# Optimization experiments

Hardware: AMD Instinct MI355X
Metric: run time of the kernel (lower is better)

Reference implementation:

```python
import jax, jax.numpy as jnp
import numpy as np

D = 1024      # embedding_dim
H = 16        # num_heads
DH = D // H   # head_dim
DFF = 4 * D
EPS = 1e-5


def setup_inputs() -> dict:
    key = jax.random.key(0)
    ks = jax.random.split(key, 10)
    B, T = 2, 2048
    s = 0.02
    return {
        "x": jax.random.normal(ks[0], (B, T, D), dtype=jnp.float32),
        "Wq": jax.random.normal(ks[1], (H, D, DH), dtype=jnp.float32) * s,
        "Wk": jax.random.normal(ks[2], (H, D, DH), dtype=jnp.float32) * s,
        "Wv": jax.random.normal(ks[3], (H, D, DH), dtype=jnp.float32) * s,
        "W1": jax.random.normal(ks[4], (D, DFF), dtype=jnp.float32) * s,
        "b1": jnp.zeros((DFF,), dtype=jnp.float32),
        "W2": jax.random.normal(ks[5], (DFF, D), dtype=jnp.float32) * s,
        "b2": jnp.zeros((D,), dtype=jnp.float32),
        "gamma1": jnp.ones((D,), dtype=jnp.float32),
        "beta1": jnp.zeros((D,), dtype=jnp.float32),
        "gamma2": jnp.ones((D,), dtype=jnp.float32),
        "beta2": jnp.zeros((D,), dtype=jnp.float32),
    }


def _layernorm(x, gamma, beta):
    # torch.var default is unbiased (ddof=1) -- faithful to LayerNorm1d
    mean = jnp.mean(x, axis=-1, keepdims=True)
    var = jnp.var(x, axis=-1, keepdims=True, ddof=1)
    return gamma * (x - mean) * jax.lax.rsqrt(var + EPS) + beta


def _block(x, Wq, Wk, Wv, W1, b1, W2, b2, gamma1, beta1, gamma2, beta2):
    B, T, _ = x.shape
    h = _layernorm(x, gamma1, beta1)
    # per-head projections stacked: [B,H,T,DH]
    Q = jnp.einsum('btd,hde->bhte', h, Wq)
    K = jnp.einsum('btd,hde->bhte', h, Wk)
    V = jnp.einsum('btd,hde->bhte', h, Wv)
    # NOTE: original scales by 1/sqrt(embedding_dim), NOT head_dim
    scores = jnp.einsum('bhqe,bhke->bhqk', Q, K) / jnp.sqrt(jnp.float32(D))
    causal = jnp.tril(jnp.ones((T, T), dtype=bool))
    scores = jnp.where(causal, scores, -jnp.inf)
    attn = jax.nn.softmax(scores, axis=-1)
    out = jnp.einsum('bhqk,bhke->bhqe', attn, V)
    # torch.cat over heads along last dim == transpose+reshape
    out = out.transpose(0, 2, 1, 3).reshape(B, T, D)
    x = x + out
    h2 = _layernorm(x, gamma2, beta2)
    ff = jax.nn.relu(h2 @ W1 + b1) @ W2 + b2  # dropout is identity at inference
    return x + ff


def reference(x, Wq, Wk, Wv, W1, b1, W2, b2, gamma1, beta1, gamma2, beta2):
    return _block(x, Wq, Wk, Wv, W1, b1, W2, b2, gamma1, beta1, gamma2, beta2)
```

## Files before the change

kernel.cpp:

```cpp
#include <hip/hip_runtime.h>

typedef unsigned short u16;
typedef __bf16 bf16;
typedef __attribute__((ext_vector_type(8))) __bf16 bf16x8;
typedef __attribute__((ext_vector_type(4))) float f32x4;
typedef __attribute__((ext_vector_type(8))) unsigned short u16x8;
typedef unsigned long long u64;

__device__ __forceinline__ float bf2f(u16 h) {
  return __uint_as_float(((unsigned int)h) << 16);
}
__device__ __forceinline__ u16 f2bf(float f) {
  unsigned int u = __float_as_uint(f);
  return (u16)((u + 0x7fffu + ((u >> 16) & 1u)) >> 16);
}
__device__ __forceinline__ u16 ld_cv(const void* p, size_t i, int f32) {
  return f32 ? f2bf(((const float*)p)[i]) : ((const u16*)p)[i];
}
__device__ __forceinline__ float ld_f(const void* p, size_t i, int f32) {
  return f32 ? ((const float*)p)[i] : bf2f(((const u16*)p)[i]);
}
__device__ __forceinline__ void async16(const u16* g, u16* l) {
  __builtin_amdgcn_global_load_lds(
      (const __attribute__((address_space(1))) unsigned int*)g,
      (__attribute__((address_space(3))) unsigned int*)l, 16, 0, 0);
}
__device__ __forceinline__ float exp2_raw(float x) {
  float r;
  asm("v_exp_f32 %0, %1" : "=v"(r) : "v"(x));
  return r;
}
__device__ __forceinline__ unsigned cvt_pk_bf16(float a, float b) {
  unsigned r;
  asm("v_cvt_pk_bf16_f32 %0, %1, %2" : "=v"(r) : "v"(a), "v"(b));
  return r;
}

__global__ void prep_kernel(const u16* __restrict__ x,
                            const void* __restrict__ Wq, const void* __restrict__ Wk,
                            const void* __restrict__ Wv, const void* __restrict__ W1,
                            const void* __restrict__ W2,
                            u16* __restrict__ WTq, u16* __restrict__ W1T,
                            u16* __restrict__ W2T,
                            const void* __restrict__ gamma1,
                            const void* __restrict__ beta1,
                            u16* __restrict__ hOut, int* __restrict__ flag) {
  __shared__ u16 tile[64][65];
  __shared__ int sm[4];
  __shared__ float ss[4], ssq[4];
  const int tid = threadIdx.x;
  int me = 0;
#pragma unroll
  for (int j = 0; j < 4; j++) {
    const u16 v = x[(tid * 4 + j) * 2];
    const int e = (v >> 7) & 0xFF;
    me = me > e ? me : e;
  }
#pragma unroll
  for (int off = 32; off > 0; off >>= 1) {
    const int o = __shfl_down(me, off);
    me = me > o ? me : o;
  }
  if ((tid & 63) == 0) sm[tid >> 6] = me;
  __syncthreads();
  const int a01 = sm[0] > sm[1] ? sm[0] : sm[1];
  const int a23 = sm[2] > sm[3] ? sm[2] : sm[3];
  const int f = ((a01 > a23 ? a01 : a23) >= 140) ? 1 : 0;
  if (blockIdx.x == 0 && tid == 0) *flag = f;

  const int bid = blockIdx.x;
  if (bid >= 2816) {
    const size_t row = bid - 2816;
    float v0, v1, v2, v3;
    if (f) {
      const float4 v = *((const float4*)x + row * 256 + tid);
      v0 = v.x; v1 = v.y; v2 = v.z; v3 = v.w;
    } else {
      const ushort4 u = *((const ushort4*)x + row * 256 + tid);
      v0 = bf2f(u.x); v1 = bf2f(u.y); v2 = bf2f(u.z); v3 = bf2f(u.w);
    }
    float s = v0 + v1 + v2 + v3;
    float sq = v0 * v0 + v1 * v1 + v2 * v2 + v3 * v3;
#pragma unroll
    for (int off = 32; off > 0; off >>= 1) {
      s += __shfl_down(s, off);
      sq += __shfl_down(sq, off);
    }
    if ((tid & 63) == 0) { ss[tid >> 6] = s; ssq[tid >> 6] = sq; }
    __syncthreads();
    s = ss[0] + ss[1] + ss[2] + ss[3];
    sq = ssq[0] + ssq[1] + ssq[2] + ssq[3];
    const float mean = s * (1.f / 1024.f);
    const float var = (sq - 1024.f * mean * mean) * (1.f / 1023.f);
    const float rs = rsqrtf(var + 1e-5f);
    const int c0 = tid * 4;
    ushort4 o;
    o.x = f2bf(ld_f(gamma1, c0 + 0, f) * (v0 - mean) * rs + ld_f(beta1, c0 + 0, f));
    o.y = f2bf(ld_f(gamma1, c0 + 1, f) * (v1 - mean) * rs + ld_f(beta1, c0 + 1, f));
    o.z = f2bf(ld_f(gamma1, c0 + 2, f) * (v2 - mean) * rs + ld_f(beta1, c0 + 2, f));
    o.w = f2bf(ld_f(gamma1, c0 + 3, f) * (v3 - mean) * rs + ld_f(beta1, c0 + 3, f));
    *(ushort4*)&hOut[row * 1024 + tid * 4] = o;
    return;
  }

  const void* src;
  u16* dst;
  int R, C, tcc, trr, rowbase;
  size_t sb = 0;
  if (bid < 768) {
    const int bx = bid & 15, wh = bid >> 4;
    const int w = wh >> 4, hh = wh & 15;
    trr = bx * 64;
    src = (w == 0) ? Wq : ((w == 1) ? Wk : Wv);
    sb = (size_t)hh * 65536;
    dst = WTq; R = 1024; C = 64; tcc = 0;
    rowbase = w * 1024 + hh * 64;
  } else if (bid < 1792) {
    const int j = bid - 768;
    src = W1; dst = W1T; R = 1024; C = 4096;
    tcc = (j & 63) * 64; trr = (j >> 6) * 64;
    rowbase = tcc;
  } else {
    const int j = bid - 1792;
    src = W2; dst = W2T; R = 4096; C = 1024;
    tcc = (j & 15) * 64; trr = (j >> 4) * 64;
    rowbase = tcc;
  }
  const int rr = tid >> 4, c4 = (tid & 15) * 4;
#pragma unroll
  for (int p = 0; p < 4; p++) {
    const int r = p * 16 + rr;
    const size_t off = sb + (size_t)(trr + r) * C + tcc + c4;
    if (f) {
      const float4 v = *(const float4*)((const float*)src + off);
      tile[r][c4 + 0] = f2bf(v.x);
      tile[r][c4 + 1] = f2bf(v.y);
      tile[r][c4 + 2] = f2bf(v.z);
      tile[r][c4 + 3] = f2bf(v.w);
    } else {
      const ushort4 u = *(const ushort4*)((const u16*)src + off);
      tile[r][c4 + 0] = u.x;
      tile[r][c4 + 1] = u.y;
      tile[r][c4 + 2] = u.z;
      tile[r][c4 + 3] = u.w;
    }
  }
  __syncthreads();
#pragma unroll
  for (int p = 0; p < 4; p++) {
    const int wrow = p * 16 + rr;
    ushort4 o;
    o.x = tile[c4 + 0][wrow];
    o.y = tile[c4 + 1][wrow];
    o.z = tile[c4 + 2][wrow];
    o.w = tile[c4 + 3][wrow];
    *(ushort4*)&dst[(size_t)(rowbase + wrow) * R + trr + c4] = o;
  }
}

template <int EPI, int WR, int WC, bool MS>
__launch_bounds__(WR * WC * 64)
__global__ void gemm_bt(const u16* __restrict__ A, const u16* __restrict__ B,
                        int K, int KLD, int NX, int N,
                        const void* __restrict__ bias, const u16* __restrict__ res,
                        void* __restrict__ out,
                        u16* __restrict__ Qo, u16* __restrict__ Ko, u16* __restrict__ Vto,
                        const int* __restrict__ flag) {
  constexpr int BM = WR * 64, BN = WC * 64, T = WR * WC * 64;
  constexpr int RPA = T / 4;
  constexpr int RAH = BM / RPA;
  constexpr int RBH = BN / RPA;
  __shared__ __align__(16) u16 As[BM * 64];
  __shared__ __align__(16) u16 Bs[BN * 64];
  const int tid = threadIdx.x;
  const int bid = blockIdx.x;
  const int sxp = NX >> 3;
  const int xcd = bid & 7, j9 = bid >> 3;
  int m0, n0;
  if (MS) {
    m0 = (xcd * sxp + j9 % sxp) * BM;
    n0 = (j9 / sxp) * BN;
  } else {
    n0 = (xcd * sxp + j9 % sxp) * BN;
    m0 = (j9 / sxp) * BM;
  }
  const int wave = tid >> 6, lane = tid & 63;
  const int wm = (wave / WC) * 64, wn = (wave % WC) * 64;
  const int lm = lane & 15, lq = lane >> 4;
  const int fb = (EPI == 1 || EPI == 2) ? *flag : 0;

  const f32x4 zero = {0.f, 0.f, 0.f, 0.f};
  f32x4 acc[4][4];
#pragma unroll
  for (int i = 0; i < 4; i++)
#pragma unroll
    for (int j = 0; j < 4; j++) acc[i][j] = zero;

  const int ar = tid >> 2;
  const int ac = ((tid & 3) ^ ((tid >> 3) & 3)) * 8;
  const u16* Ag = A + (size_t)(m0 + ar) * KLD + ac;
  const u16* Bg = B + (size_t)(n0 + ar) * KLD + ac;
  u16* AsP = &As[tid * 8];
  u16* BsP = &Bs[tid * 8];
  const int rq = (lq ^ ((lm >> 1) & 3)) * 8;

  for (int k0 = 0; k0 < K; k0 += 64) {
#pragma unroll
    for (int hh = 0; hh < 2; hh++) {
#pragma unroll
      for (int c = 0; c < RAH; c++)
        async16(Ag + k0 + hh * 32 + (size_t)c * RPA * KLD,
                AsP + hh * BM * 32 + c * RPA * 32);
#pragma unroll
      for (int c = 0; c < RBH; c++)
        async16(Bg + k0 + hh * 32 + (size_t)c * RPA * KLD,
                BsP + hh * BN * 32 + c * RPA * 32);
    }
    __syncthreads();
    bf16x8 a0[4], a1[4], b0[4], b1[4];
#pragma unroll
    for (int i = 0; i < 4; i++) {
      a0[i] = *(const bf16x8*)&As[(wm + i * 16 + lm) * 32 + rq];
      a1[i] = *(const bf16x8*)&As[BM * 32 + (wm + i * 16 + lm) * 32 + rq];
    }
#pragma unroll
    for (int i = 0; i < 4; i++) {
      b0[i] = *(const bf16x8*)&Bs[(wn + i * 16 + lm) * 32 + rq];
      b1[i] = *(const bf16x8*)&Bs[BN * 32 + (wn + i * 16 + lm) * 32 + rq];
    }
#pragma unroll
    for (int i = 0; i < 4; i++)
#pragma unroll
      for (int j = 0; j < 4; j++) {
        acc[i][j] = __builtin_amdgcn_mfma_f32_16x16x32_bf16(a0[i], b0[j], acc[i][j], 0, 0, 0);
        acc[i][j] = __builtin_amdgcn_mfma_f32_16x16x32_bf16(a1[i], b1[j], acc[i][j], 0, 0, 0);
      }
    __syncthreads();
  }

  if (EPI == 0) {
#pragma unroll
    for (int i = 0; i < 4; i++) {
      const int row0 = m0 + wm + i * 16 + lq * 4;
      const int bb = row0 >> 11, t0 = row0 & 2047;
#pragma unroll
      for (int j = 0; j < 4; j++) {
        const int col = n0 + wn + j * 16 + lm;
        const int w = col >> 10, nn = col & 1023;
        const int hh = nn >> 6, e = nn & 63;
        if (w == 2) {
          ushort4 v4;
          v4.x = f2bf(acc[i][j][0]);
          v4.y = f2bf(acc[i][j][1]);
          v4.z = f2bf(acc[i][j][2]);
          v4.w = f2bf(acc[i][j][3]);
          *(ushort4*)&Vto[(((size_t)(bb * 16 + hh)) * 64 + e) * 2048 + t0] = v4;
        } else {
          u16* dst = (w == 0) ? Qo : Ko;
          const float qs = (w == 0) ? 0.04508422f : 1.0f;
#pragma unroll
          for (int r = 0; r < 4; r++)
            dst[(((size_t)(bb * 16 + hh)) * 2048 + t0 + r) * 64 + e] =
                f2bf(acc[i][j][r] * qs);
        }
      }
    }
  } else {
#pragma unroll
    for (int i = 0; i < 4; i++) {
#pragma unroll
      for (int r = 0; r < 4; r++) {
        const int row = m0 + wm + i * 16 + lq * 4 + r;
#pragma unroll
        for (int j = 0; j < 4; j++) {
          const int col = n0 + wn + j * 16 + lm;
          const float c = acc[i][j][r];
          if (EPI == 1) {
            const float v = c + ld_f(bias, col, fb);
            ((u16*)out)[(size_t)row * N + col] = f2bf(v > 0.f ? v : 0.f);
          } else {
            const float v = c + ld_f(bias, col, fb) + bf2f(res[(size_t)row * N + col]);
            if (fb)
              ((float*)out)[(size_t)row * N + col] = v;
            else
              ((u16*)out)[(size_t)row * N + col] = f2bf(v);
          }
        }
      }
    }
  }
}

__launch_bounds__(512)
__global__ void gemm_sk2(const u16* __restrict__ A, const u16* __restrict__ B,
                         u16* __restrict__ P0, u16* __restrict__ P1) {
  __shared__ __align__(16) unsigned char smem[66560];
  const int tid = threadIdx.x;
  const int bid = blockIdx.x;
  const int xcd = bid & 7, j9 = bid >> 3;
  const int m0 = (xcd * 4 + (j9 & 3)) * 128;
  const int n0 = ((j9 >> 2) & 7) * 128;
  const int khb = (j9 >> 5) & 1;
  const int wave = tid >> 6, lane = tid & 63;
  const int g = wave >> 2, lw = wave & 3;
  const int gtid = tid & 255;
  const int wm = (lw >> 1) * 64, wn = (lw & 1) * 64;
  const int lm = lane & 15, lq = lane >> 4;

  const f32x4 zero = {0.f, 0.f, 0.f, 0.f};
  f32x4 acc[4][4];
#pragma unroll
  for (int i = 0; i < 4; i++)
#pragma unroll
    for (int j = 0; j < 4; j++) acc[i][j] = zero;

  const int ar = gtid >> 2;
  const int ac = ((gtid & 3) ^ ((gtid >> 3) & 3)) * 8;
  const int koff = khb * 2048 + g * 1024;
  const u16* Ag = A + (size_t)(m0 + ar) * 4096 + koff + ac;
  const u16* Bg = B + (size_t)(n0 + ar) * 4096 + koff + ac;
  u16* Sg = (u16*)smem + g * 16384;
  u16* AsP = &Sg[gtid * 8];
  u16* BsP = &Sg[8192 + gtid * 8];
  const int rq = (lq ^ ((lm >> 1) & 3)) * 8;

  for (int k0 = 0; k0 < 1024; k0 += 64) {
#pragma unroll
    for (int hh = 0; hh < 2; hh++) {
#pragma unroll
      for (int c = 0; c < 2; c++) {
        async16(Ag + k0 + hh * 32 + (size_t)c * 64 * 4096,
                AsP + hh * 4096 + c * 2048);
        async16(Bg + k0 + hh * 32 + (size_t)c * 64 * 4096,
                BsP + hh * 4096 + c * 2048);
      }
    }
    __syncthreads();
    bf16x8 a0[4], a1[4], b0[4], b1[4];
#pragma unroll
    for (int i = 0; i < 4; i++) {
      a0[i] = *(const bf16x8*)&Sg[(wm + i * 16 + lm) * 32 + rq];
      a1[i] = *(const bf16x8*)&Sg[4096 + (wm + i * 16 + lm) * 32 + rq];
    }
#pragma unroll
    for (int i = 0; i < 4; i++) {
      b0[i] = *(const bf16x8*)&Sg[8192 + (wn + i * 16 + lm) * 32 + rq];
      b1[i] = *(const bf16x8*)&Sg[8192 + 4096 + (wn + i * 16 + lm) * 32 + rq];
    }
#pragma unroll
    for (int i = 0; i < 4; i++)
#pragma unroll
      for (int j = 0; j < 4; j++) {
        acc[i][j] = __builtin_amdgcn_mfma_f32_16x16x32_bf16(a0[i], b0[j], acc[i][j], 0, 0, 0);
        acc[i][j] = __builtin_amdgcn_mfma_f32_16x16x32_bf16(a1[i], b1[j], acc[i][j], 0, 0, 0);
      }
    __syncthreads();
  }

  float* Ml = (float*)smem;
  if (g == 1) {
#pragma unroll
    for (int i = 0; i < 4; i++)
#pragma unroll
      for (int j = 0; j < 4; j++)
#pragma unroll
        for (int r = 0; r < 4; r++)
          Ml[(wm + i * 16 + lq * 4 + r) * 130 + wn + j * 16 + lm] = acc[i][j][r];
  }
  __syncthreads();
  if (g == 0) {
    u16* P = khb ? P1 : P0;
#pragma unroll
    for (int i = 0; i < 4; i++) {
#pragma unroll
      for (int r = 0; r < 4; r++) {
        const int row = m0 + wm + i * 16 + lq * 4 + r;
#pragma unroll
        for (int j = 0; j < 4; j++) {
          const int col = n0 + wn + j * 16 + lm;
          const float v = acc[i][j][r] +
                          Ml[(wm + i * 16 + lq * 4 + r) * 130 + wn + j * 16 + lm];
          P[(size_t)row * 1024 + col] = f2bf(v);
        }
      }
    }
  }
}

__launch_bounds__(256)
__global__ void ffn2_reduce(const u16* __restrict__ P0, const u16* __restrict__ P1,
                            const void* __restrict__ bias, const u16* __restrict__ res,
                            void* __restrict__ out, const int* __restrict__ flag) {
  const int f = *flag;
  const size_t i0 = ((size_t)blockIdx.x * 256 + threadIdx.x) * 8;
  const int col = (int)(i0 & 1023);
  const u16x8 a8 = *(const u16x8*)(P0 + i0);
  const u16x8 b8 = *(const u16x8*)(P1 + i0);
  const u16x8 r8 = *(const u16x8*)(res + i0);
  float v[8];
#pragma unroll
  for (int k = 0; k < 8; k++)
    v[k] = bf2f(a8[k]) + bf2f(b8[k]) + ld_f(bias, col + k, f) + bf2f(r8[k]);
  if (f) {
    float4 o0 = {v[0], v[1], v[2], v[3]};
    float4 o1 = {v[4], v[5], v[6], v[7]};
    *(float4*)((float*)out + i0) = o0;
    *(float4*)((float*)out + i0 + 4) = o1;
  } else {
    u16x8 o8;
#pragma unroll
    for (int k = 0; k < 8; k++) o8[k] = f2bf(v[k]);
    *(u16x8*)((u16*)out + i0) = o8;
  }
}

__launch_bounds__(256)
__global__ void attn_mfma(const u16* __restrict__ Q, const u16* __restrict__ K,
                          const u16* __restrict__ Vt, const void* __restrict__ xres,
                          const int* __restrict__ flag, u16* __restrict__ x2) {
  __shared__ __align__(16) unsigned char smem[35328];
  const int tid = threadIdx.x;
  const int wave = tid >> 6, lane = tid & 63;
  const int lm = lane & 15, quad = lane >> 4;
  const int bid = blockIdx.x;
  const int xcd = bid & 7, jj = bid >> 3;
  const int bh = xcd + 8 * (jj & 3);
  const int pair = jj >> 2;
  const int b = bh >> 4, h = bh & 15;
  const int f32in = *flag;

  u16* stw = (u16*)smem + wave * 4096;
  u16* Ksw = stw;
  u16* Vsw = stw + 2048;
  float (*Olds)[32][68] = (float(*)[32][68])smem;
  float (*Llds)[2][16] = (float(*)[2][16])(smem + 34816);

  const u16* Kbh = K + (size_t)bh * 131072;
  const u16* Vbh = Vt + (size_t)bh * 131072;
  const f32x4 zero = {0.f, 0.f, 0.f, 0.f};
  const int srow = lane >> 2;
  const int sch2 = (((lane & 3) ^ ((srow >> 1) & 3))) * 8;
  const int rk = (lm >> 1) & 3;

  union V8 { bf16x8 v; struct { u64 lo, hi; } q; };
  u16x8 ob;
#pragma unroll
  for (int k = 0; k < 8; k++) ob[k] = 0x3F80;
  const bf16x8 ones = *(const bf16x8*)&ob;

  auto stageK = [&](int t) {
    const int ks = t * 32;
#pragma unroll
    for (int hh2 = 0; hh2 < 2; hh2++)
#pragma unroll
      for (int c = 0; c < 2; c++)
        async16(Kbh + (size_t)(ks + c * 16 + srow) * 64 + hh2 * 32 + sch2,
                Ksw + hh2 * 1024 + c * 512 + lane * 8);
  };
  auto stageV = [&](int t) {
    const int ks = t * 32;
#pragma unroll
    for (int c = 0; c < 4; c++)
      async16(Vbh + (size_t)(c * 16 + srow) * 2048 + ks + sch2,
              Vsw + c * 512 + lane * 8);
  };

#pragma unroll 1
  for (int phase = 0; phase < 2; phase++) {
    const int qb = phase ? (63 - pair) : pair;
    const int qw0 = qb * 32;

    bf16x8 qf[2][2];
#pragma unroll
    for (int s = 0; s < 2; s++) {
      const u16* Qp = Q + ((size_t)bh * 2048 + qw0 + s * 16 + lm) * 64 + quad * 8;
      qf[s][0] = *(const bf16x8*)Qp;
      qf[s][1] = *(const bf16x8*)(Qp + 32);
    }
    __builtin_amdgcn_s_waitcnt(0x0F70);
    f32x4 ot[2][4];
    f32x4 al[2];
#pragma unroll
    for (int s = 0; s < 2; s++) {
#pragma unroll
      for (int j = 0; j < 4; j++) ot[s][j] = zero;
      al[s] = zero;
    }

    const int nt = qb + 1;
    const int si = (nt * wave) >> 2;
    const int ei = (nt * (wave + 1)) >> 2;

    if (si < ei) { stageK(si); stageV(si); }

#pragma unroll 1
    for (int t = si; t < ei; t++) {
      asm volatile("s_waitcnt vmcnt(4)" ::: "memory");
      bf16x8 kk[2][2];
#pragma unroll
      for (int hh = 0; hh < 2; hh++) {
        kk[hh][0] = *(const bf16x8*)&Ksw[(hh * 16 + lm) * 32 + (quad ^ rk) * 8];
        kk[hh][1] = *(const bf16x8*)&Ksw[1024 + (hh * 16 + lm) * 32 + (quad ^ rk) * 8];
      }
      f32x4 S[2][2];
#pragma unroll
      for (int s = 0; s < 2; s++)
#pragma unroll
        for (int hh = 0; hh < 2; hh++) {
          f32x4 a = zero;
          a = __builtin_amdgcn_mfma_f32_16x16x32_bf16(kk[hh][0], qf[s][0], a, 0, 0, 0);
          a = __builtin_amdgcn_mfma_f32_16x16x32_bf16(kk[hh][1], qf[s][1], a, 0, 0, 0);
          S[s][hh] = a;
        }
      __builtin_amdgcn_sched_barrier(0);
      const bool more = (t + 1 < ei);
      if (more) {
        stageK(t + 1);
        asm volatile("s_waitcnt vmcnt(4)" ::: "memory");
      } else {
        asm volatile("s_waitcnt vmcnt(0)" ::: "memory");
      }
      V8 vf[4];
#pragma unroll
      for (int j = 0; j < 4; j++) {
        vf[j].q.lo = *(const u64*)&Vsw[(j * 16 + lm) * 32 +
                                       (((quad >> 1)) ^ rk) * 8 + (quad & 1) * 4];
        vf[j].q.hi = *(const u64*)&Vsw[(j * 16 + lm) * 32 +
                                       (((quad >> 1) | 2) ^ rk) * 8 + (quad & 1) * 4];
      }
      const bool maskT = (t == qb);
#pragma unroll
      for (int s = 0; s < 2; s++) {
        float p[2][4];
#pragma unroll
        for (int hh = 0; hh < 2; hh++)
#pragma unroll
          for (int r = 0; r < 4; r++)
            p[hh][r] = exp2_raw(S[s][hh][r]);
        if (maskT) {
#pragma unroll
          for (int hh = 0; hh < 2; hh++)
#pragma unroll
            for (int r = 0; r < 4; r++)
              if (hh * 16 + quad * 4 + r > s * 16 + lm) p[hh][r] = 0.f;
        }
        unsigned pk[4];
        pk[0] = cvt_pk_bf16(p[0][0], p[0][1]);
        pk[1] = cvt_pk_bf16(p[0][2], p[0][3]);
        pk[2] = cvt_pk_bf16(p[1][0], p[1][1]);
        pk[3] = cvt_pk_bf16(p[1][2], p[1][3]);
        const bf16x8 pf = *(const bf16x8*)pk;
        al[s] = __builtin_amdgcn_mfma_f32_16x16x32_bf16(ones, pf, al[s], 0, 0, 0);
#pragma unroll
        for (int j = 0; j < 4; j++)
          ot[s][j] = __builtin_amdgcn_mfma_f32_16x16x32_bf16(vf[j].v, pf, ot[s][j], 0, 0, 0);
      }
      __builtin_amdgcn_sched_barrier(0);
      if (more) stageV(t + 1);
    }

    __syncthreads();

#pragma unroll
    for (int s = 0; s < 2; s++)
#pragma unroll
      for (int j = 0; j < 4; j++)
        *(f32x4*)&Olds[wave][s * 16 + lm][j * 16 + quad * 4] = ot[s][j];
    if (quad == 0) {
      Llds[wave][0][lm] = al[0][0];
      Llds[wave][1][lm] = al[1][0];
    }
    __syncthreads();
    const int q = tid >> 3;
    const int e0 = (tid & 7) * 8;
    f32x4 oa = zero, obv = zero;
#pragma unroll
    for (int w = 0; w < 4; w++) {
      oa += *(const f32x4*)&Olds[w][q][e0];
      obv += *(const f32x4*)&Olds[w][q][e0 + 4];
    }
    const float lt = Llds[0][q >> 4][q & 15] + Llds[1][q >> 4][q & 15] +
                     Llds[2][q >> 4][q & 15] + Llds[3][q >> 4][q & 15];
    const float linv = 1.f / lt;
    const size_t rowbase = ((size_t)(b * 2048 + qw0 + q)) * 1024 + h * 64 + e0;
    float xv[8];
    if (f32in) {
      const float* xf = (const float*)xres + rowbase;
      const float4 u0 = *(const float4*)xf;
      const float4 u1 = *(const float4*)(xf + 4);
      xv[0] = u0.x; xv[1] = u0.y; xv[2] = u0.z; xv[3] = u0.w;
      xv[4] = u1.x; xv[5] = u1.y; xv[6] = u1.z; xv[7] = u1.w;
    } else {
      const u16x8 u = *(const u16x8*)((const u16*)xres + rowbase);
#pragma unroll
      for (int k = 0; k < 8; k++) xv[k] = bf2f(u[k]);
    }
    u16x8 o8;
#pragma unroll
    for (int k = 0; k < 4; k++) o8[k] = f2bf(xv[k] + oa[k] * linv);
#pragma unroll
    for (int k = 0; k < 4; k++) o8[4 + k] = f2bf(xv[4 + k] + obv[k] * linv);
    *(u16x8*)&x2[rowbase] = o8;
    __syncthreads();
  }
}

__launch_bounds__(256)
__global__ void ln_kernel(const void* __restrict__ x, const void* __restrict__ gamma,
                          const void* __restrict__ beta, u16* __restrict__ out,
                          const int* __restrict__ flag, int xraw) {
  const size_t row = blockIdx.x;
  const int tid = threadIdx.x;
  const int f = *flag;
  const int fx = xraw ? f : 0;
  float v0, v1, v2, v3;
  if (fx) {
    const float4 v = *((const float4*)x + row * 256 + tid);
    v0 = v.x; v1 = v.y; v2 = v.z; v3 = v.w;
  } else {
    const ushort4 u = *((const ushort4*)x + row * 256 + tid);
    v0 = bf2f(u.x); v1 = bf2f(u.y); v2 = bf2f(u.z); v3 = bf2f(u.w);
  }
  float s = v0 + v1 + v2 + v3;
  float sq = v0 * v0 + v1 * v1 + v2 * v2 + v3 * v3;
#pragma unroll
  for (int off = 32; off > 0; off >>= 1) {
    s += __shfl_down(s, off);
    sq += __shfl_down(sq, off);
  }
  __shared__ float ss[4], ssq[4];
  if ((tid & 63) == 0) { ss[tid >> 6] = s; ssq[tid >> 6] = sq; }
  __syncthreads();
  s = ss[0] + ss[1] + ss[2] + ss[3];
  sq = ssq[0] + ssq[1] + ssq[2] + ssq[3];
  const float mean = s * (1.f / 1024.f);
  const float var = (sq - 1024.f * mean * mean) * (1.f / 1023.f);
  const float rs = rsqrtf(var + 1e-5f);
  const int c0 = tid * 4;
  ushort4 o;
  o.x = f2bf(ld_f(gamma, c0 + 0, f) * (v0 - mean) * rs + ld_f(beta, c0 + 0, f));
  o.y = f2bf(ld_f(gamma, c0 + 1, f) * (v1 - mean) * rs + ld_f(beta, c0 + 1, f));
  o.z = f2bf(ld_f(gamma, c0 + 2, f) * (v2 - mean) * rs + ld_f(beta, c0 + 2, f));
  o.w = f2bf(ld_f(gamma, c0 + 3, f) * (v3 - mean) * rs + ld_f(beta, c0 + 3, f));
  *(ushort4*)&out[row * 1024 + tid * 4] = o;
}

extern "C" void kernel_launch(void* const* d_in, const int* in_sizes, int n_in,
                              void* d_out, int out_size, void* d_ws, size_t ws_size,
                              hipStream_t stream) {
  const void* x      = d_in[0];
  const void* Wq     = d_in[1];
  const void* Wk     = d_in[2];
  const void* Wv     = d_in[3];
  const void* W1     = d_in[4];
  const void* b1     = d_in[5];
  const void* W2     = d_in[6];
  const void* b2     = d_in[7];
  const void* gamma1 = d_in[8];
  const void* beta1  = d_in[9];
  const void* gamma2 = d_in[10];
  const void* beta2  = d_in[11];
  u16* ws = (u16*)d_ws;

  const size_t M4 = 4194304;
  u16* h   = ws;
  u16* Qb  = ws + 1 * M4;
  u16* Kb  = ws + 2 * M4;
  u16* Vtb = ws + 3 * M4;
  u16* WTq = ws + 4 * M4;
  u16* x2  = ws + 4 * M4;
  u16* h2  = ws + 5 * M4;
  u16* W1T = ws + 6 * M4;
  u16* W2T = ws + 7 * M4;
  u16* ff1 = ws;
  u16* P0  = ws + 5 * M4;
  u16* P1  = ws + 6 * M4;
  int* flag = (int*)(ws + 8 * M4 + 9216);

  prep_kernel<<<6912, 256, 0, stream>>>((const u16*)x, Wq, Wk, Wv, W1, W2,
                                        WTq, W1T, W2T, gamma1, beta1, h, flag);
  gemm_bt<0, 2, 2, false><<<768, 256, 0, stream>>>(h, WTq, 1024, 1024, 24, 3072,
                                                   nullptr, nullptr, nullptr,
                                                   Qb, Kb, Vtb, flag);
  attn_mfma<<<1024, 256, 0, stream>>>(Qb, Kb, Vtb, x, flag, x2);
  ln_kernel<<<4096, 256, 0, stream>>>(x2, gamma2, beta2, h2, flag, 0);
  gemm_bt<1, 4, 2, false><<<512, 512, 0, stream>>>(h2, W1T, 1024, 1024, 32, 4096,
                                                   b1, nullptr, ff1,
                                                   nullptr, nullptr, nullptr, flag);
  gemm_sk2<<<512, 512, 0, stream>>>(ff1, W2T, P0, P1);
  ffn2_reduce<<<2048, 256, 0, stream>>>(P0, P1, b2, x2, d_out, flag);
}
```

Before: 311.5 us.

## Run QKV projection with the intra-block split-K two-group GEMM kernel

The QKV projection GEMM (M=4096, N=3072, K=1024) moves from the 128x128-tile-per-64-row gemm_bt with 256 threads to a generalized split-K kernel. It uses 512 threads, where two wave groups each cover half of K on a 128x128 tile and combine their partial sums through LDS. The FFN2 split-K kernel is folded into the same template. The aim is higher per-block occupancy and larger tiles for QKV, at the cost of an extra LDS reduction and a shorter K loop per group.

```diff
diff --git a/kernel.cpp b/kernel.cpp
--- a/kernel.cpp
+++ b/kernel.cpp
@@ -163,9 +163,7 @@
 __global__ void gemm_bt(const u16* __restrict__ A, const u16* __restrict__ B,
                         int K, int KLD, int NX, int N,
                         const void* __restrict__ bias, const u16* __restrict__ res,
-                        void* __restrict__ out,
-                        u16* __restrict__ Qo, u16* __restrict__ Ko, u16* __restrict__ Vto,
-                        const int* __restrict__ flag) {
+                        void* __restrict__ out, const int* __restrict__ flag) {
   constexpr int BM = WR * 64, BN = WC * 64, T = WR * WC * 64;
   constexpr int RPA = T / 4;
   constexpr int RAH = BM / RPA;
@@ -238,69 +236,50 @@
     __syncthreads();
   }
 
-  if (EPI == 0) {
-#pragma unroll
-    for (int i = 0; i < 4; i++) {
-      const int row0 = m0 + wm + i * 16 + lq * 4;
-      const int bb = row0 >> 11, t0 = row0 & 2047;
+#pragma unroll
+  for (int i = 0; i < 4; i++) {
+#pragma unroll
+    for (int r = 0; r < 4; r++) {
+      const int row = m0 + wm + i * 16 + lq * 4 + r;
 #pragma unroll
       for (int j = 0; j < 4; j++) {
         const int col = n0 + wn + j * 16 + lm;
-        const int w = col >> 10, nn = col & 1023;
-        const int hh = nn >> 6, e = nn & 63;
-        if (w == 2) {
-          ushort4 v4;
-          v4.x = f2bf(acc[i][j][0]);
-          v4.y = f2bf(acc[i][j][1]);
-          v4.z = f2bf(acc[i][j][2]);
-          v4.w = f2bf(acc[i][j][3]);
-          *(ushort4*)&Vto[(((size_t)(bb * 16 + hh)) * 64 + e) * 2048 + t0] = v4;
+        const float c = acc[i][j][r];
+        if (EPI == 1) {
+          const float v = c + ld_f(bias, col, fb);
+          ((u16*)out)[(size_t)row * N + col] = f2bf(v > 0.f ? v : 0.f);
         } else {
-          u16* dst = (w == 0) ? Qo : Ko;
-          const float qs = (w == 0) ? 0.04508422f : 1.0f;
-#pragma unroll
-          for (int r = 0; r < 4; r++)
-            dst[(((size_t)(bb * 16 + hh)) * 2048 + t0 + r) * 64 + e] =
-                f2bf(acc[i][j][r] * qs);
+          const float v = c + ld_f(bias, col, fb) + bf2f(res[(size_t)row * N + col]);
+          if (fb)
+            ((float*)out)[(size_t)row * N + col] = v;
+          else
+            ((u16*)out)[(size_t)row * N + col] = f2bf(v);
         }
       }
     }
-  } else {
-#pragma unroll
-    for (int i = 0; i < 4; i++) {
-#pragma unroll
-      for (int r = 0; r < 4; r++) {
-        const int row = m0 + wm + i * 16 + lq * 4 + r;
-#pragma unroll
-        for (int j = 0; j < 4; j++) {
-          const int col = n0 + wn + j * 16 + lm;
-          const float c = acc[i][j][r];
-          if (EPI == 1) {
-            const float v = c + ld_f(bias, col, fb);
-            ((u16*)out)[(size_t)row * N + col] = f2bf(v > 0.f ? v : 0.f);
-          } else {
-            const float v = c + ld_f(bias, col, fb) + bf2f(res[(size_t)row * N + col]);
-            if (fb)
-              ((float*)out)[(size_t)row * N + col] = v;
-            else
-              ((u16*)out)[(size_t)row * N + col] = f2bf(v);
-          }
-        }
-      }
-    }
-  }
-}
-
+  }
+}
+
+template <int EPI>
 __launch_bounds__(512)
-__global__ void gemm_sk2(const u16* __restrict__ A, const u16* __restrict__ B,
-                         u16* __restrict__ P0, u16* __restrict__ P1) {
+__global__ void gemm_dg(const u16* __restrict__ A, const u16* __restrict__ B,
+                        u16* __restrict__ O0, u16* __restrict__ O1,
+                        u16* __restrict__ O2) {
   __shared__ __align__(16) unsigned char smem[66560];
   const int tid = threadIdx.x;
   const int bid = blockIdx.x;
   const int xcd = bid & 7, j9 = bid >> 3;
-  const int m0 = (xcd * 4 + (j9 & 3)) * 128;
-  const int n0 = ((j9 >> 2) & 7) * 128;
-  const int khb = (j9 >> 5) & 1;
+  int m0, n0, koff, KH, KLD, khb = 0;
+  if (EPI == 0) {
+    n0 = (xcd * 3 + j9 % 3) * 128;
+    m0 = (j9 / 3) * 128;
+    KH = 512; KLD = 1024; koff = 0;
+  } else {
+    m0 = (xcd * 4 + (j9 & 3)) * 128;
+    n0 = ((j9 >> 2) & 7) * 128;
+    khb = (j9 >> 5) & 1;
+    KH = 1024; KLD = 4096; koff = khb * 2048;
+  }
   const int wave = tid >> 6, lane = tid & 63;
   const int g = wave >> 2, lw = wave & 3;
   const int gtid = tid & 255;
@@ -316,22 +295,22 @@
 
   const int ar = gtid >> 2;
   const int ac = ((gtid & 3) ^ ((gtid >> 3) & 3)) * 8;
-  const int koff = khb * 2048 + g * 1024;
-  const u16* Ag = A + (size_t)(m0 + ar) * 4096 + koff + ac;
-  const u16* Bg = B + (size_t)(n0 + ar) * 4096 + koff + ac;
+  koff += g * KH;
+  const u16* Ag = A + (size_t)(m0 + ar) * KLD + koff + ac;
+  const u16* Bg = B + (size_t)(n0 + ar) * KLD + koff + ac;
   u16* Sg = (u16*)smem + g * 16384;
   u16* AsP = &Sg[gtid * 8];
   u16* BsP = &Sg[8192 + gtid * 8];
   const int rq = (lq ^ ((lm >> 1) & 3)) * 8;
 
-  for (int k0 = 0; k0 < 1024; k0 += 64) {
+  for (int k0 = 0; k0 < KH; k0 += 64) {
 #pragma unroll
     for (int hh = 0; hh < 2; hh++) {
 #pragma unroll
       for (int c = 0; c < 2; c++) {
-        async16(Ag + k0 + hh * 32 + (size_t)c * 64 * 4096,
+        async16(Ag + k0 + hh * 32 + (size_t)c * 64 * KLD,
                 AsP + hh * 4096 + c * 2048);
-        async16(Bg + k0 + hh * 32 + (size_t)c * 64 * 4096,
+        async16(Bg + k0 + hh * 32 + (size_t)c * 64 * KLD,
                 BsP + hh * 4096 + c * 2048);
       }
     }
@@ -369,18 +348,52 @@
   }
   __syncthreads();
   if (g == 0) {
-    u16* P = khb ? P1 : P0;
-#pragma unroll
-    for (int i = 0; i < 4; i++) {
-#pragma unroll
-      for (int r = 0; r < 4; r++) {
-        const int row = m0 + wm + i * 16 + lq * 4 + r;
+    if (EPI == 0) {
+#pragma unroll
+      for (int i = 0; i < 4; i++) {
+        const int row0 = m0 + wm + i * 16 + lq * 4;
+        const int bb = row0 >> 11, t0 = row0 & 2047;
 #pragma unroll
         for (int j = 0; j < 4; j++) {
           const int col = n0 + wn + j * 16 + lm;
-          const float v = acc[i][j][r] +
-                          Ml[(wm + i * 16 + lq * 4 + r) * 130 + wn + j * 16 + lm];
-          P[(size_t)row * 1024 + col] = f2bf(v);
+          const int w = col >> 10, nn = col & 1023;
+          const int hh = nn >> 6, e = nn & 63;
+          float vm[4];
+#pragma unroll
+          for (int r = 0; r < 4; r++)
+            vm[r] = acc[i][j][r] +
+                    Ml[(wm + i * 16 + lq * 4 + r) * 130 + wn + j * 16 + lm];
+          if (w == 2) {
+            ushort4 v4;
+            v4.x = f2bf(vm[0]);
+            v4.y = f2bf(vm[1]);
+            v4.z = f2bf(vm[2]);
+            v4.w = f2bf(vm[3]);
+            *(ushort4*)&O2[(((size_t)(bb * 16 + hh)) * 64 + e) * 2048 + t0] = v4;
+          } else {
+            u16* dst = (w == 0) ? O0 : O1;
+            const float qs = (w == 0) ? 0.04508422f : 1.0f;
+#pragma unroll
+            for (int r = 0; r < 4; r++)
+              dst[(((size_t)(bb * 16 + hh)) * 2048 + t0 + r) * 64 + e] =
+                  f2bf(vm[r] * qs);
+          }
+        }
+      }
+    } else {
+      u16* P = khb ? O1 : O0;
+#pragma unroll
+      for (int i = 0; i < 4; i++) {
+#pragma unroll
+        for (int r = 0; r < 4; r++) {
+          const int row = m0 + wm + i * 16 + lq * 4 + r;
+#pragma unroll
+          for (int j = 0; j < 4; j++) {
+            const int col = n0 + wn + j * 16 + lm;
+            const float v = acc[i][j][r] +
+                            Ml[(wm + i * 16 + lq * 4 + r) * 130 + wn + j * 16 + lm];
+            P[(size_t)row * 1024 + col] = f2bf(v);
+          }
         }
       }
     }
@@ -679,14 +692,11 @@
 
   prep_kernel<<<6912, 256, 0, stream>>>((const u16*)x, Wq, Wk, Wv, W1, W2,
                                         WTq, W1T, W2T, gamma1, beta1, h, flag);
-  gemm_bt<0, 2, 2, false><<<768, 256, 0, stream>>>(h, WTq, 1024, 1024, 24, 3072,
-                                                   nullptr, nullptr, nullptr,
-                                                   Qb, Kb, Vtb, flag);
+  gemm_dg<0><<<768, 512, 0, stream>>>(h, WTq, Qb, Kb, Vtb);
   attn_mfma<<<1024, 256, 0, stream>>>(Qb, Kb, Vtb, x, flag, x2);
   ln_kernel<<<4096, 256, 0, stream>>>(x2, gamma2, beta2, h2, flag, 0);
   gemm_bt<1, 4, 2, false><<<512, 512, 0, stream>>>(h2, W1T, 1024, 1024, 32, 4096,
-                                                   b1, nullptr, ff1,
-                                                   nullptr, nullptr, nullptr, flag);
-  gemm_sk2<<<512, 512, 0, stream>>>(ff1, W2T, P0, P1);
+                                                   b1, nullptr, ff1, flag);
+  gemm_dg<3><<<512, 512, 0, stream>>>(ff1, W2T, P0, P1, nullptr);
   ffn2_reduce<<<2048, 256, 0, stream>>>(P0, P1, b2, x2, d_out, flag);
 }
```

After: 317.9 us. 2.0% more time.
